# Optimization experiments

Measured on AMD Instinct MI355X. Metric: run time of the kernel, lower is better.

## Reference

```python
import jax, jax.numpy as jnp
import numpy as np

EPS = 1e-8
FUSION_THRESHOLD = 0.95
N, D = 8192, 256
NUM_CATEGORIES = 80


def setup_inputs() -> dict:
    key = jax.random.key(0)
    k1, k2, k3 = jax.random.split(key, 3)
    return {
        "kernels": jax.random.normal(k1, (1, N, D), dtype=jnp.float32),
        "categories": jax.random.randint(k2, (1, N), 0, NUM_CATEGORIES, dtype=jnp.int64),
        "scores": jax.random.uniform(k3, (1, N), dtype=jnp.float32),
    }


def reference(kernels, categories, scores):
    # squeeze batch (module asserts batch == 1)
    k = kernels[0]          # [N, D]
    c = categories[0]       # [N]
    s = scores[0]           # [N]

    # CosineSelfSimilarity: normalize rows (norm computed in float32, clamped at eps)
    nrm = jnp.maximum(
        jnp.linalg.norm(k.astype(jnp.float32), axis=1, keepdims=True), EPS
    )
    a_norm = k / nrm
    sim = a_norm @ a_norm.T                                  # [N, N]

    # upper-triangular threshold mask (diagonal included, matches torch.triu)
    label = jnp.triu(sim) >= FUSION_THRESHOLD
    # category gating (mask_categories=True)
    label = label & (c[:, None] == c[None, :])

    # greedy cumsum dedup: a kernel survives iff its column has < 2 hits so far
    cum = jnp.cumsum(label.astype(jnp.float32), axis=0) < 2.0  # [N, N] bool
    keep = jnp.diagonal(cum)                                   # [N] bool

    # In the original, rows are boolean-selected by `keep` (dynamic shape).
    # For jit compatibility we keep shape [N] and zero out dropped rows.
    label_f = (label & cum & keep[:, None]).astype(jnp.float32)  # [N, N]
    label_norm = jnp.sum(label_f, axis=1, keepdims=True)          # [N, 1]
    # kept rows always include the diagonal => norm >= 1; clamp for dropped rows
    fused = (label_f @ k) / jnp.maximum(label_norm, 1.0)          # [N, D]

    cats_out = jnp.where(keep, c, -1)
    scores_out = jnp.where(keep, s, 0.0)
    return fused[None], cats_out[None], scores_out[None], keep[None]
```

## Files before the change

### kernel.cpp

```cpp
#include <hip/hip_runtime.h>
#include <cstdint>

#define NROWS 8192
#define DDIM  256
#define THR   0.95f
#define EPSN  1e-8f
#define IMAX  0x7FFFFFFF
#define NCAT  80
#define MAXT  16

typedef unsigned short u16;
typedef short v8s __attribute__((ext_vector_type(8)));
typedef float v4f __attribute__((ext_vector_type(4)));

__device__ __forceinline__ u16 f2b(float f) {
    union { float f; unsigned int i; } v; v.f = f;
    if ((v.i & 0x7F800000u) == 0x7F800000u) {
        return (u16)((v.i >> 16) | ((v.i & 0xFFFFu) ? 0x40 : 0));
    }
    unsigned int r = v.i + 0x7FFFu + ((v.i >> 16) & 1u);
    return (u16)(r >> 16);
}

__global__ __launch_bounds__(256) void k_norm_sort(const float* __restrict__ kin,
                                                   const int* __restrict__ cat,
                                                   u16* __restrict__ anorm,
                                                   int* __restrict__ sortedRows,
                                                   int* __restrict__ catBase,
                                                   int* __restrict__ mergeCnt) {
    const int t = threadIdx.x;
    if (blockIdx.x < NROWS / 4) {
        const int w = t >> 6, l = t & 63;
        const int row = (blockIdx.x << 2) + w;
        const float4 v = ((const float4*)(kin + (size_t)row * DDIM))[l];
        float s = v.x * v.x + v.y * v.y + v.z * v.z + v.w * v.w;
        for (int o = 32; o >= 1; o >>= 1) s += __shfl_xor(s, o);
        const float rn = 1.0f / fmaxf(sqrtf(s), EPSN);
        ushort4 o4;
        o4.x = f2b(v.x * rn); o4.y = f2b(v.y * rn);
        o4.z = f2b(v.z * rn); o4.w = f2b(v.w * rn);
        ((ushort4*)(anorm + (size_t)row * DDIM))[l] = o4;
        return;
    }
    __shared__ u16 h[NCAT][256];
    __shared__ int tot[NCAT];
    __shared__ int base[NCAT + 1];
    for (int i = t; i < NCAT * 256; i += 256) ((u16*)h)[i] = 0;
    __syncthreads();
    {
        const int r0 = t << 5;
        for (int k = 0; k < 32; ++k) h[cat[r0 + k]][t]++;
    }
    __syncthreads();
    if (t < NCAT) {
        int s = 0;
        for (int q = 0; q < 256; ++q) s += (int)h[t][q];
        tot[t] = s;
    }
    __syncthreads();
    if (t == 0) {
        int run = 0;
        for (int c = 0; c < NCAT; ++c) { base[c] = run; run += tot[c]; }
        base[NCAT] = run;
        *mergeCnt = 0;
    }
    __syncthreads();
    if (t <= NCAT) catBase[t] = base[t];
    if (t < NCAT) {
        int run = 0;
        for (int q = 0; q < 256; ++q) { const int v = (int)h[t][q]; h[t][q] = (u16)run; run += v; }
    }
    __syncthreads();
    {
        const int r0 = t << 5;
        for (int k = 0; k < 32; ++k) {
            const int r = r0 + k, c = cat[r];
            const int rel = (int)h[c][t]++;
            sortedRows[base[c] + rel] = r;
        }
    }
}

__global__ __launch_bounds__(256) void k_hits_cat(const u16* __restrict__ anorm,
                                                  const float* __restrict__ sc,
                                                  const int* __restrict__ sortedRows,
                                                  const int* __restrict__ catBase,
                                                  int* __restrict__ hit1,
                                                  int* __restrict__ hit2,
                                                  int* __restrict__ mergeCnt,
                                                  int* __restrict__ mergeList,
                                                  float* __restrict__ out) {
    const int c  = blockIdx.x >> 4;
    const int ct = blockIdx.x & 15;
    const int nbase = catBase[c];
    const int nc = catBase[c + 1] - nbase;
    const int ncT = (nc + 15) >> 4;
    if (ct >= ncT) return;
    const int* lst = sortedRows + nbase;

    __shared__ int colH1[16];
    const int t = threadIdx.x;
    if (t < 16) colH1[t] = IMAX;
    __syncthreads();

    const int wv = t >> 6, l = t & 63;
    const int lo16 = l & 15, quad = l >> 4;

    const int qloc = (ct << 4) + lo16;
    const int gq = lst[qloc < nc ? qloc : nc - 1];
    const u16* qrow = anorm + ((size_t)gq << 8) + (quad << 3);
    v8s bfr[8];
#pragma unroll
    for (int kk = 0; kk < 8; ++kk) bfr[kk] = *(const v8s*)(qrow + (kk << 5));

    for (int rt = wv; rt <= ct; rt += 4) {
        const int ploc = (rt << 4) + lo16;
        const int gp = lst[ploc < nc ? ploc : nc - 1];
        const u16* prow = anorm + ((size_t)gp << 8) + (quad << 3);
        v4f acc = {0.f, 0.f, 0.f, 0.f};
#pragma unroll
        for (int kk = 0; kk < 8; ++kk) {
            const v8s af = *(const v8s*)(prow + (kk << 5));
            acc = __builtin_amdgcn_mfma_f32_16x16x32_bf16(af, bfr[kk], acc, 0, 0, 0);
        }
#pragma unroll
        for (int reg = 0; reg < 4; ++reg) {
            const int p = (rt << 4) + (quad << 2) + reg;
            if (acc[reg] >= THR && p < qloc && qloc < nc) atomicMin(&colH1[lo16], p);
        }
    }
    __syncthreads();

    if (t < 16) {
        const int q = (ct << 4) + t;
        if (q < nc) {
            const int g = lst[q];
            const int h1p = colH1[t];
            const bool hasHit = (h1p != IMAX);
            hit1[g] = hasHit ? lst[h1p] : g;
            hit2[g] = hasHit ? 0 : IMAX;
            float* cats  = out + (size_t)NROWS * DDIM;
            float* scso  = cats + NROWS;
            float* keepo = scso + NROWS;
            cats[g]  = hasHit ? -1.0f : (float)c;
            scso[g]  = hasHit ? 0.0f : sc[g];
            keepo[g] = hasHit ? 0.0f : 1.0f;
            if (hasHit) mergeList[atomicAdd(mergeCnt, 1)] = g;
        }
    }
}

__global__ __launch_bounds__(256) void k_out(const float* __restrict__ kin,
                                             const int* __restrict__ hit1,
                                             const int* __restrict__ hit2,
                                             const int* __restrict__ mergeCnt,
                                             const int* __restrict__ mergeList,
                                             float* __restrict__ out) {
    const int t = threadIdx.x, l = t & 63;
    const int i = (int)(blockIdx.x << 2) + (t >> 6);
    const bool keep = (hit2[i] == IMAX);

    float ax = 0.f, ay = 0.f, az = 0.f, aw = 0.f;
    if (keep) {
        const float4 v = ((const float4*)(kin + (size_t)i * DDIM))[l];
        ax = v.x; ay = v.y; az = v.z; aw = v.w;
        int cnt = 1;
        const int mc = *mergeCnt;
        for (int q = 0; q < mc; q++) {
            const int jr = mergeList[q];
            if (hit1[jr] == i) {
                const float4 b = ((const float4*)(kin + (size_t)jr * DDIM))[l];
                ax += b.x; ay += b.y; az += b.z; aw += b.w; cnt++;
            }
        }
        const float fc = (float)cnt;
        ax /= fc; ay /= fc; az /= fc; aw /= fc;
    }
    float4 o4; o4.x = ax; o4.y = ay; o4.z = az; o4.w = aw;
    ((float4*)(out + (size_t)i * DDIM))[l] = o4;
}

extern "C" void kernel_launch(void* const* d_in, const int* in_sizes, int n_in,
                              void* d_out, int out_size, void* d_ws, size_t ws_size,
                              hipStream_t stream) {
    (void)in_sizes; (void)n_in; (void)out_size; (void)ws_size;
    const float* kin = (const float*)d_in[0];
    const int*   cat = (const int*)d_in[1];
    const float* sc  = (const float*)d_in[2];
    float* out = (float*)d_out;

    char* ws = (char*)d_ws;
    u16* anorm      = (u16*)ws;
    int* hit1       = (int*)(ws + (size_t)NROWS * DDIM * 2);
    int* hit2       = hit1 + NROWS;
    int* sortedRows = hit2 + NROWS;
    int* catBase    = sortedRows + NROWS;
    int* mergeCnt   = catBase + 128;
    int* mergeList  = mergeCnt + 16;

    k_norm_sort<<<NROWS / 4 + 1, 256, 0, stream>>>(kin, cat, anorm, sortedRows,
                                                   catBase, mergeCnt);
    k_hits_cat<<<NCAT * MAXT, 256, 0, stream>>>(anorm, sc, sortedRows, catBase,
                                                hit1, hit2, mergeCnt, mergeList, out);
    k_out<<<NROWS / 4, 256, 0, stream>>>(kin, hit1, hit2, mergeCnt, mergeList, out);
}
```

Before: 94.94 us.

## Fuse category sort, hit detection and output into one per-category kernel

Replaces the global sort, per-tile hit kernel and per-row output kernel with one block per category. Each block scans the category array with a prefix sum to build its own row list, computes the similarity tiles, keeps first-hit indices in shared memory and writes the fused rows directly. This drops a kernel launch and the workspace round trips for hit arrays and the merge list. In exchange only 80 blocks run, which leaves most CUs idle, and each block must scan all 8192 categories. Categories with more than 256 rows are silently truncated.

```diff
diff --git a/kernel.cpp b/kernel.cpp
--- a/kernel.cpp
+++ b/kernel.cpp
@@ -7,7 +7,7 @@
 #define EPSN  1e-8f
 #define IMAX  0x7FFFFFFF
 #define NCAT  80
-#define MAXT  16
+#define MAXC  256
 
 typedef unsigned short u16;
 typedef short v8s __attribute__((ext_vector_type(8)));
@@ -22,162 +22,121 @@
     return (u16)(r >> 16);
 }
 
-__global__ __launch_bounds__(256) void k_norm_sort(const float* __restrict__ kin,
-                                                   const int* __restrict__ cat,
-                                                   u16* __restrict__ anorm,
-                                                   int* __restrict__ sortedRows,
-                                                   int* __restrict__ catBase,
-                                                   int* __restrict__ mergeCnt) {
-    const int t = threadIdx.x;
-    if (blockIdx.x < NROWS / 4) {
-        const int w = t >> 6, l = t & 63;
-        const int row = (blockIdx.x << 2) + w;
-        const float4 v = ((const float4*)(kin + (size_t)row * DDIM))[l];
-        float s = v.x * v.x + v.y * v.y + v.z * v.z + v.w * v.w;
-        for (int o = 32; o >= 1; o >>= 1) s += __shfl_xor(s, o);
-        const float rn = 1.0f / fmaxf(sqrtf(s), EPSN);
-        ushort4 o4;
-        o4.x = f2b(v.x * rn); o4.y = f2b(v.y * rn);
-        o4.z = f2b(v.z * rn); o4.w = f2b(v.w * rn);
-        ((ushort4*)(anorm + (size_t)row * DDIM))[l] = o4;
-        return;
-    }
-    __shared__ u16 h[NCAT][256];
-    __shared__ int tot[NCAT];
-    __shared__ int base[NCAT + 1];
-    for (int i = t; i < NCAT * 256; i += 256) ((u16*)h)[i] = 0;
-    __syncthreads();
-    {
-        const int r0 = t << 5;
-        for (int k = 0; k < 32; ++k) h[cat[r0 + k]][t]++;
-    }
-    __syncthreads();
-    if (t < NCAT) {
-        int s = 0;
-        for (int q = 0; q < 256; ++q) s += (int)h[t][q];
-        tot[t] = s;
-    }
-    __syncthreads();
-    if (t == 0) {
-        int run = 0;
-        for (int c = 0; c < NCAT; ++c) { base[c] = run; run += tot[c]; }
-        base[NCAT] = run;
-        *mergeCnt = 0;
-    }
-    __syncthreads();
-    if (t <= NCAT) catBase[t] = base[t];
-    if (t < NCAT) {
-        int run = 0;
-        for (int q = 0; q < 256; ++q) { const int v = (int)h[t][q]; h[t][q] = (u16)run; run += v; }
-    }
-    __syncthreads();
-    {
-        const int r0 = t << 5;
-        for (int k = 0; k < 32; ++k) {
-            const int r = r0 + k, c = cat[r];
-            const int rel = (int)h[c][t]++;
-            sortedRows[base[c] + rel] = r;
-        }
-    }
+__global__ __launch_bounds__(256) void k_norm(const float* __restrict__ kin,
+                                              u16* __restrict__ anorm) {
+    const int t = threadIdx.x, w = t >> 6, l = t & 63;
+    const int row = (blockIdx.x << 2) + w;
+    const float4 v = ((const float4*)(kin + (size_t)row * DDIM))[l];
+    float s = v.x * v.x + v.y * v.y + v.z * v.z + v.w * v.w;
+    for (int o = 32; o >= 1; o >>= 1) s += __shfl_xor(s, o);
+    const float rn = 1.0f / fmaxf(sqrtf(s), EPSN);
+    ushort4 o4;
+    o4.x = f2b(v.x * rn); o4.y = f2b(v.y * rn);
+    o4.z = f2b(v.z * rn); o4.w = f2b(v.w * rn);
+    ((ushort4*)(anorm + (size_t)row * DDIM))[l] = o4;
 }
 
-__global__ __launch_bounds__(256) void k_hits_cat(const u16* __restrict__ anorm,
-                                                  const float* __restrict__ sc,
-                                                  const int* __restrict__ sortedRows,
-                                                  const int* __restrict__ catBase,
-                                                  int* __restrict__ hit1,
-                                                  int* __restrict__ hit2,
-                                                  int* __restrict__ mergeCnt,
-                                                  int* __restrict__ mergeList,
-                                                  float* __restrict__ out) {
-    const int c  = blockIdx.x >> 4;
-    const int ct = blockIdx.x & 15;
-    const int nbase = catBase[c];
-    const int nc = catBase[c + 1] - nbase;
-    const int ncT = (nc + 15) >> 4;
-    if (ct >= ncT) return;
-    const int* lst = sortedRows + nbase;
-
-    __shared__ int colH1[16];
+__global__ __launch_bounds__(256) void k_cat(const u16* __restrict__ anorm,
+                                             const float* __restrict__ kin,
+                                             const int* __restrict__ cat,
+                                             const float* __restrict__ sc,
+                                             float* __restrict__ out) {
+    const int c = blockIdx.x;
     const int t = threadIdx.x;
-    if (t < 16) colH1[t] = IMAX;
-    __syncthreads();
-
     const int wv = t >> 6, l = t & 63;
     const int lo16 = l & 15, quad = l >> 4;
 
-    const int qloc = (ct << 4) + lo16;
-    const int gq = lst[qloc < nc ? qloc : nc - 1];
-    const u16* qrow = anorm + ((size_t)gq << 8) + (quad << 3);
-    v8s bfr[8];
+    __shared__ int lst[MAXC];
+    __shared__ int colH1[MAXC];
+    __shared__ int psum[256];
+    __shared__ int mlist[MAXC];
+    __shared__ int mcnt_s, nc_s;
+
+    {
+        const int r0 = t << 5;
+        int cnt = 0;
+        for (int k = 0; k < 32; ++k) cnt += (cat[r0 + k] == c);
+        psum[t] = cnt;
+        __syncthreads();
+        for (int off = 1; off < 256; off <<= 1) {
+            const int v = (t >= off) ? psum[t - off] : 0;
+            __syncthreads();
+            psum[t] += v;
+            __syncthreads();
+        }
+        int pos = psum[t] - cnt;
+        if (t == 255) { nc_s = psum[255] < MAXC ? psum[255] : MAXC; mcnt_s = 0; }
+        for (int k = 0; k < 32; ++k) {
+            const int r = r0 + k;
+            if (cat[r] == c) { if (pos < MAXC) lst[pos] = r; ++pos; }
+        }
+    }
+    colH1[t] = IMAX;
+    __syncthreads();
+    const int nc = nc_s;
+    const int ncT = (nc + 15) >> 4;
+
+    for (int ct = wv; ct < ncT; ct += 4) {
+        const int qloc = (ct << 4) + lo16;
+        const int gq = lst[qloc < nc ? qloc : nc - 1];
+        const u16* qrow = anorm + ((size_t)gq << 8) + (quad << 3);
+        v8s bfr[8];
 #pragma unroll
-    for (int kk = 0; kk < 8; ++kk) bfr[kk] = *(const v8s*)(qrow + (kk << 5));
+        for (int kk = 0; kk < 8; ++kk) bfr[kk] = *(const v8s*)(qrow + (kk << 5));
 
-    for (int rt = wv; rt <= ct; rt += 4) {
-        const int ploc = (rt << 4) + lo16;
-        const int gp = lst[ploc < nc ? ploc : nc - 1];
-        const u16* prow = anorm + ((size_t)gp << 8) + (quad << 3);
-        v4f acc = {0.f, 0.f, 0.f, 0.f};
+        for (int rt = 0; rt <= ct; ++rt) {
+            const int ploc = (rt << 4) + lo16;
+            const int gp = lst[ploc < nc ? ploc : nc - 1];
+            const u16* prow = anorm + ((size_t)gp << 8) + (quad << 3);
+            v4f acc = {0.f, 0.f, 0.f, 0.f};
 #pragma unroll
-        for (int kk = 0; kk < 8; ++kk) {
-            const v8s af = *(const v8s*)(prow + (kk << 5));
-            acc = __builtin_amdgcn_mfma_f32_16x16x32_bf16(af, bfr[kk], acc, 0, 0, 0);
-        }
+            for (int kk = 0; kk < 8; ++kk) {
+                const v8s af = *(const v8s*)(prow + (kk << 5));
+                acc = __builtin_amdgcn_mfma_f32_16x16x32_bf16(af, bfr[kk], acc, 0, 0, 0);
+            }
 #pragma unroll
-        for (int reg = 0; reg < 4; ++reg) {
-            const int p = (rt << 4) + (quad << 2) + reg;
-            if (acc[reg] >= THR && p < qloc && qloc < nc) atomicMin(&colH1[lo16], p);
+            for (int reg = 0; reg < 4; ++reg) {
+                const int p = (rt << 4) + (quad << 2) + reg;
+                if (acc[reg] >= THR && p < qloc && qloc < nc) atomicMin(&colH1[lo16 + (ct << 4)], p);
+            }
         }
     }
     __syncthreads();
 
-    if (t < 16) {
-        const int q = (ct << 4) + t;
-        if (q < nc) {
-            const int g = lst[q];
-            const int h1p = colH1[t];
-            const bool hasHit = (h1p != IMAX);
-            hit1[g] = hasHit ? lst[h1p] : g;
-            hit2[g] = hasHit ? 0 : IMAX;
-            float* cats  = out + (size_t)NROWS * DDIM;
-            float* scso  = cats + NROWS;
-            float* keepo = scso + NROWS;
-            cats[g]  = hasHit ? -1.0f : (float)c;
-            scso[g]  = hasHit ? 0.0f : sc[g];
-            keepo[g] = hasHit ? 0.0f : 1.0f;
-            if (hasHit) mergeList[atomicAdd(mergeCnt, 1)] = g;
+    if (t < nc && colH1[t] != IMAX) mlist[atomicAdd(&mcnt_s, 1)] = t;
+    __syncthreads();
+    const int mc = mcnt_s;
+
+    float* cats  = out + (size_t)NROWS * DDIM;
+    float* scso  = cats + NROWS;
+    float* keepo = scso + NROWS;
+    if (t < nc) {
+        const int g = lst[t];
+        const bool keep = (colH1[t] == IMAX);
+        cats[g]  = keep ? (float)c : -1.0f;
+        scso[g]  = keep ? sc[g] : 0.0f;
+        keepo[g] = keep ? 1.0f : 0.0f;
+    }
+
+    for (int i = wv; i < nc; i += 4) {
+        const int g = lst[i];
+        float4 o4 = {0.f, 0.f, 0.f, 0.f};
+        if (colH1[i] == IMAX) {
+            const float4 v = ((const float4*)(kin + ((size_t)g << 8)))[l];
+            float ax = v.x, ay = v.y, az = v.z, aw = v.w;
+            int cnt = 1;
+            for (int k = 0; k < mc; ++k) {
+                const int q = mlist[k];
+                if (colH1[q] == i) {
+                    const float4 b = ((const float4*)(kin + ((size_t)lst[q] << 8)))[l];
+                    ax += b.x; ay += b.y; az += b.z; aw += b.w; ++cnt;
+                }
+            }
+            const float fc = (float)cnt;
+            o4.x = ax / fc; o4.y = ay / fc; o4.z = az / fc; o4.w = aw / fc;
         }
+        ((float4*)(out + ((size_t)g << 8)))[l] = o4;
     }
-}
-
-__global__ __launch_bounds__(256) void k_out(const float* __restrict__ kin,
-                                             const int* __restrict__ hit1,
-                                             const int* __restrict__ hit2,
-                                             const int* __restrict__ mergeCnt,
-                                             const int* __restrict__ mergeList,
-                                             float* __restrict__ out) {
-    const int t = threadIdx.x, l = t & 63;
-    const int i = (int)(blockIdx.x << 2) + (t >> 6);
-    const bool keep = (hit2[i] == IMAX);
-
-    float ax = 0.f, ay = 0.f, az = 0.f, aw = 0.f;
-    if (keep) {
-        const float4 v = ((const float4*)(kin + (size_t)i * DDIM))[l];
-        ax = v.x; ay = v.y; az = v.z; aw = v.w;
-        int cnt = 1;
-        const int mc = *mergeCnt;
-        for (int q = 0; q < mc; q++) {
-            const int jr = mergeList[q];
-            if (hit1[jr] == i) {
-                const float4 b = ((const float4*)(kin + (size_t)jr * DDIM))[l];
-                ax += b.x; ay += b.y; az += b.z; aw += b.w; cnt++;
-            }
-        }
-        const float fc = (float)cnt;
-        ax /= fc; ay /= fc; az /= fc; aw /= fc;
-    }
-    float4 o4; o4.x = ax; o4.y = ay; o4.z = az; o4.w = aw;
-    ((float4*)(out + (size_t)i * DDIM))[l] = o4;
 }
 
 extern "C" void kernel_launch(void* const* d_in, const int* in_sizes, int n_in,
@@ -189,18 +148,8 @@
     const float* sc  = (const float*)d_in[2];
     float* out = (float*)d_out;
 
-    char* ws = (char*)d_ws;
-    u16* anorm      = (u16*)ws;
-    int* hit1       = (int*)(ws + (size_t)NROWS * DDIM * 2);
-    int* hit2       = hit1 + NROWS;
-    int* sortedRows = hit2 + NROWS;
-    int* catBase    = sortedRows + NROWS;
-    int* mergeCnt   = catBase + 128;
-    int* mergeList  = mergeCnt + 16;
+    u16* anorm = (u16*)d_ws;
 
-    k_norm_sort<<<NROWS / 4 + 1, 256, 0, stream>>>(kin, cat, anorm, sortedRows,
-                                                   catBase, mergeCnt);
-    k_hits_cat<<<NCAT * MAXT, 256, 0, stream>>>(anorm, sc, sortedRows, catBase,
-                                                hit1, hit2, mergeCnt, mergeList, out);
-    k_out<<<NROWS / 4, 256, 0, stream>>>(kin, hit1, hit2, mergeCnt, mergeList, out);
+    k_norm<<<NROWS / 4, 256, 0, stream>>>(kin, anorm);
+    k_cat<<<NCAT, 256, 0, stream>>>(anorm, kin, cat, sc, out);
 }
```

New measurement: 96.69 us. About the same (+1.8%).
